# Kernel optimization log

Hardware: AMD Instinct MI355X
Metric: run time of the kernel (lower is better)

The kernel has to match this reference:

```python
import jax, jax.numpy as jnp
import numpy as np
import math

B, S, H, E, D = 4, 4096, 2048, 64, 256
ROUND_COUNT = 3
TARGET_APPLIED_FRACTION = 0.25


def setup_inputs() -> dict:
    key = jax.random.key(0)
    ks = jax.random.split(key, 10)
    sc = 0.02
    return {
        "hidden": jax.random.normal(ks[0], (B, S, H), jnp.float32),
        "W_ts": jax.random.normal(ks[1], (D, H), jnp.float32) * sc,
        "b_ts": jnp.zeros((D,), jnp.float32),
        "W_tr": jax.random.normal(ks[2], (E, H), jnp.float32) * sc,
        "b_tr": jnp.zeros((E,), jnp.float32),
        "W_sr": jax.random.normal(ks[3], (E, D), jnp.float32) * sc,
        "W_fb": jax.random.normal(ks[4], (D, E), jnp.float32) * sc,
        "W_r": jax.random.normal(ks[5], (D, D), jnp.float32) * sc,
        "b_r": jnp.zeros((D,), jnp.float32),
        "W_z": jax.random.normal(ks[6], (D, D), jnp.float32) * sc,
        "b_z": jnp.zeros((D,), jnp.float32),
        "W_ci": jax.random.normal(ks[7], (D, D), jnp.float32) * sc,
        "b_ci": jnp.zeros((D,), jnp.float32),
        "W_cs": jax.random.normal(ks[8], (D, D), jnp.float32) * sc,
    }


def _lowest_margin_fraction_mask(route_weights, frac):
    # winner margin: top1 - top2 over experts
    top2 = jax.lax.top_k(route_weights, 2)[0]          # [B,S,2]
    margins = top2[..., 0] - top2[..., 1]              # [B,S]
    flat = margins.reshape(-1)
    n = flat.shape[0]
    k = min(n, max(1, math.ceil(frac * n)))            # static count
    order = jnp.argsort(flat, stable=True)
    active = jnp.zeros((n,), jnp.bool_).at[order[:k]].set(True)
    return active.reshape(margins.shape)


def reference(hidden, W_ts, b_ts, W_tr, b_tr, W_sr, W_fb, W_r, b_r, W_z, b_z, W_ci, b_ci, W_cs):
    # token state + base route logits
    token_state = jnp.tanh(hidden @ W_ts.T + b_ts)          # [B,S,D]
    pooled_token_state = token_state.mean(axis=1, keepdims=True)  # [B,1,D]
    base_logits = hidden @ W_tr.T + b_tr                    # [B,S,E]

    controller = jnp.zeros((hidden.shape[0], 1, W_ts.shape[0]), hidden.dtype)  # [B,1,D]

    expert_logits = base_logits
    expert_weights = jax.nn.softmax(expert_logits, axis=-1)

    for round_index in range(ROUND_COUNT):
        if round_index > 0:
            # margin-gated conditional per-token update
            active = _lowest_margin_fraction_mask(expert_weights, TARGET_APPLIED_FRACTION)  # [B,S]
            state_route_bias = controller @ W_sr.T           # [B,1,E]
            candidate_logits = base_logits + state_route_bias
            expert_logits = jnp.where(active[..., None], candidate_logits, expert_logits)
            expert_weights = jax.nn.softmax(expert_logits, axis=-1)
        # GRU-style controller state update from pooled route feedback
        pooled_feedback = expert_weights.mean(axis=1, keepdims=True) @ W_fb.T  # [B,1,D]
        state_input = pooled_token_state + pooled_feedback
        reset_gate = jax.nn.sigmoid(state_input @ W_r.T + b_r)
        update_gate = jax.nn.sigmoid(state_input @ W_z.T + b_z)
        candidate_state = jnp.tanh(state_input @ W_ci.T + b_ci + (reset_gate * controller) @ W_cs.T)
        controller = (1.0 - update_gate) * controller + update_gate * candidate_state

    return expert_weights
```

## Files before the change

### kernel.cpp

```cpp
#include <hip/hip_runtime.h>
#include <hip/hip_bf16.h>
#include <math.h>

typedef unsigned int uint;
typedef unsigned short ushort_t;
typedef unsigned char uchar;

typedef __attribute__((ext_vector_type(4))) float f4_t;
typedef __attribute__((ext_vector_type(4))) ushort_t u16x4_t;
typedef __attribute__((ext_vector_type(4))) uint u32x4_t;
typedef __attribute__((ext_vector_type(8))) short bfrag_t;
typedef __attribute__((ext_vector_type(4))) float facc_t;

#define K_DIM 2048
#define D_DIM 256
#define E_DIM 64
#define N_DIM 320
#define S_DIM 4096
#define NTOK 16384
#define KSEL 4096

__device__ __forceinline__ ushort_t f2bf(float f) {
  uint u = __float_as_uint(f);
  uint r = u + 0x7FFFu + ((u >> 16) & 1u);
  return (ushort_t)(r >> 16);
}

__global__ __launch_bounds__(256) void prep_kernel(
    const float* __restrict__ W_ts, const float* __restrict__ W_tr,
    ushort_t* __restrict__ Wc, float* __restrict__ zero_region)
{
  int idx = blockIdx.x * 256 + threadIdx.x;
  if (idx < (N_DIM * K_DIM / 4)) {
    int n = idx >> 9;
    int k4 = (idx & 511) * 4;
    const float* src = (n < D_DIM) ? (W_ts + (size_t)n * K_DIM + k4)
                                   : (W_tr + (size_t)(n - D_DIM) * K_DIM + k4);
    f4_t v = *reinterpret_cast<const f4_t*>(src);
    u16x4_t h;
    h[0] = f2bf(v[0]); h[1] = f2bf(v[1]); h[2] = f2bf(v[2]); h[3] = f2bf(v[3]);
    *reinterpret_cast<u16x4_t*>(&Wc[(size_t)n * K_DIM + k4]) = h;
  }
  if (blockIdx.x == 0) {
    for (int i = threadIdx.x; i < 2560; i += 256) zero_region[i] = 0.f;
  }
}

#define BM 64
#define BK 64
#define LDK 72

__global__ __launch_bounds__(640, 2) void gemm_kernel(
    const float* __restrict__ hidden, const ushort_t* __restrict__ Wc,
    const float* __restrict__ b_ts, const float* __restrict__ b_tr,
    float* __restrict__ base_logits, float* __restrict__ pooled_ts)
{
  __shared__ ushort_t Alds[BM * LDK];
  __shared__ ushort_t Blds[N_DIM * LDK];
  const int tid = threadIdx.x;
  const int lane = tid & 63;
  const int w = tid >> 6;
  const int wc = w % 5;
  const int wrr = w / 5;
  const int row0 = blockIdx.x * BM;
  const int lr = lane & 15;
  const int lgp = lane >> 4;
  const bool hasA2 = (tid < 384);

  const int ar0 = tid >> 4, ac0 = (tid & 15) * 4;
  const int ar1 = (tid + 640) >> 4, ac1 = ((tid + 640) & 15) * 4;

  facc_t acc[2][4];
#pragma unroll
  for (int mi = 0; mi < 2; mi++)
#pragma unroll
    for (int ni = 0; ni < 4; ni++) acc[mi][ni] = (facc_t){0.f, 0.f, 0.f, 0.f};

  f4_t vaA0, vaA1;
  u32x4_t vb0_0, vb0_1, vb0_2, vb0_3;
  f4_t vaB0, vaB1;
  u32x4_t vb1_0, vb1_1, vb1_2, vb1_3;

#define LOAD_TILE(k0, vA0, vA1, b0, b1, b2, b3)                                  \
  {                                                                              \
    vA0 = *reinterpret_cast<const f4_t*>(hidden + (size_t)(row0 + ar0) * K_DIM + (k0) + ac0); \
    if (hasA2)                                                                   \
      vA1 = *reinterpret_cast<const f4_t*>(hidden + (size_t)(row0 + ar1) * K_DIM + (k0) + ac1); \
    b0 = *reinterpret_cast<const u32x4_t*>(Wc + (size_t)(tid >> 3) * K_DIM + (k0) + (tid & 7) * 8); \
    b1 = *reinterpret_cast<const u32x4_t*>(Wc + (size_t)((tid + 640) >> 3) * K_DIM + (k0) + ((tid + 640) & 7) * 8); \
    b2 = *reinterpret_cast<const u32x4_t*>(Wc + (size_t)((tid + 1280) >> 3) * K_DIM + (k0) + ((tid + 1280) & 7) * 8); \
    b3 = *reinterpret_cast<const u32x4_t*>(Wc + (size_t)((tid + 1920) >> 3) * K_DIM + (k0) + ((tid + 1920) & 7) * 8); \
  }

#define STORE_TILE(vA0, vA1, b0, b1, b2, b3)                                     \
  {                                                                              \
    u16x4_t h;                                                                   \
    h[0] = f2bf(vA0[0]); h[1] = f2bf(vA0[1]); h[2] = f2bf(vA0[2]); h[3] = f2bf(vA0[3]); \
    *reinterpret_cast<u16x4_t*>(&Alds[ar0 * LDK + ac0]) = h;                     \
    if (hasA2) {                                                                 \
      h[0] = f2bf(vA1[0]); h[1] = f2bf(vA1[1]); h[2] = f2bf(vA1[2]); h[3] = f2bf(vA1[3]); \
      *reinterpret_cast<u16x4_t*>(&Alds[ar1 * LDK + ac1]) = h;                   \
    }                                                                            \
    *reinterpret_cast<u32x4_t*>(&Blds[(tid >> 3) * LDK + (tid & 7) * 8]) = b0;   \
    *reinterpret_cast<u32x4_t*>(&Blds[((tid + 640) >> 3) * LDK + ((tid + 640) & 7) * 8]) = b1; \
    *reinterpret_cast<u32x4_t*>(&Blds[((tid + 1280) >> 3) * LDK + ((tid + 1280) & 7) * 8]) = b2; \
    *reinterpret_cast<u32x4_t*>(&Blds[((tid + 1920) >> 3) * LDK + ((tid + 1920) & 7) * 8]) = b3; \
  }

#define COMPUTE_TILE()                                                           \
  {                                                                              \
    _Pragma("unroll")                                                            \
    for (int kk = 0; kk < 2; ++kk) {                                             \
      bfrag_t af[2], bfv[4];                                                     \
      _Pragma("unroll")                                                          \
      for (int mi = 0; mi < 2; mi++)                                             \
        af[mi] = *reinterpret_cast<const bfrag_t*>(&Alds[(wrr * 32 + mi * 16 + lr) * LDK + kk * 32 + lgp * 8]); \
      _Pragma("unroll")                                                          \
      for (int ni = 0; ni < 4; ni++)                                             \
        bfv[ni] = *reinterpret_cast<const bfrag_t*>(&Blds[(wc * 64 + ni * 16 + lr) * LDK + kk * 32 + lgp * 8]); \
      _Pragma("unroll")                                                          \
      for (int mi = 0; mi < 2; mi++)                                             \
        _Pragma("unroll")                                                        \
        for (int ni = 0; ni < 4; ni++)                                           \
          acc[mi][ni] = __builtin_amdgcn_mfma_f32_16x16x32_bf16(af[mi], bfv[ni], acc[mi][ni], 0, 0, 0); \
    }                                                                            \
  }

  LOAD_TILE(0, vaA0, vaA1, vb0_0, vb0_1, vb0_2, vb0_3);

#pragma unroll 1
  for (int t = 0; t < 32; t += 2) {
    __syncthreads();
    STORE_TILE(vaA0, vaA1, vb0_0, vb0_1, vb0_2, vb0_3);
    LOAD_TILE((t + 1) * BK, vaB0, vaB1, vb1_0, vb1_1, vb1_2, vb1_3);
    __syncthreads();
    COMPUTE_TILE();

    __syncthreads();
    STORE_TILE(vaB0, vaB1, vb1_0, vb1_1, vb1_2, vb1_3);
    if (t + 2 < 32) LOAD_TILE((t + 2) * BK, vaA0, vaA1, vb0_0, vb0_1, vb0_2, vb0_3);
    __syncthreads();
    COMPUTE_TILE();
  }

  const int b = row0 >> 12;
  if (wc < 4) {
#pragma unroll
    for (int ni = 0; ni < 4; ni++) {
      const int col = wc * 64 + ni * 16 + lr;
      const float bias = b_ts[col];
      float psum = 0.f;
#pragma unroll
      for (int mi = 0; mi < 2; mi++)
#pragma unroll
        for (int j = 0; j < 4; j++)
          psum += tanhf(acc[mi][ni][j] + bias);
      psum += __shfl_xor(psum, 16, 64);
      psum += __shfl_xor(psum, 32, 64);
      if (lgp == 0) atomicAdd(&pooled_ts[b * D_DIM + col], psum);
    }
  } else {
#pragma unroll
    for (int ni = 0; ni < 4; ni++) {
      const int e = ni * 16 + lr;
      const float bias = b_tr[e];
#pragma unroll
      for (int mi = 0; mi < 2; mi++)
#pragma unroll
        for (int j = 0; j < 4; j++) {
          const int row = row0 + wrr * 32 + mi * 16 + lgp * 4 + j;
          base_logits[(size_t)row * E_DIM + e] = acc[mi][ni][j] + bias;
        }
    }
  }
}

__global__ __launch_bounds__(256) void route_kernel(
    int round,
    const float* __restrict__ base_logits,
    const float* __restrict__ bias1, const float* __restrict__ bias2,
    const uchar* __restrict__ active, uchar* __restrict__ tag,
    float* __restrict__ margins, float* __restrict__ pw_out,
    float* __restrict__ out)
{
  __shared__ float sm[4][64];
  const int tid = threadIdx.x;
  const int lane = tid & 63;
  const int wid = tid >> 6;
  const int b = blockIdx.x >> 8;
  const int t0 = blockIdx.x * 16 + wid * 4;

  float bv1 = 0.f, bv2 = 0.f;
  if (round >= 1) bv1 = bias1[b * E_DIM + lane];
  if (round == 2) bv2 = bias2[b * E_DIM + lane];

  float lg[4];
#pragma unroll
  for (int i = 0; i < 4; ++i)
    lg[i] = base_logits[(size_t)(t0 + i) * E_DIM + lane];

  if (round == 1) {
    uchar a[4];
#pragma unroll
    for (int i = 0; i < 4; ++i) a[i] = active[t0 + i];
#pragma unroll
    for (int i = 0; i < 4; ++i) {
      if (lane == 0) tag[t0 + i] = a[i];
      if (a[i]) lg[i] += bv1;
    }
  } else if (round == 2) {
    uchar a[4], tg[4];
#pragma unroll
    for (int i = 0; i < 4; ++i) { a[i] = active[t0 + i]; tg[i] = tag[t0 + i]; }
#pragma unroll
    for (int i = 0; i < 4; ++i)
      lg[i] += a[i] ? bv2 : (tg[i] ? bv1 : 0.f);
  }

  float pacc = 0.f;
#pragma unroll
  for (int i = 0; i < 4; ++i) {
    const float lgt = lg[i];
    float m1 = lgt;
#pragma unroll
    for (int mm = 32; mm; mm >>= 1) m1 = fmaxf(m1, __shfl_xor(m1, mm, 64));
    float e = expf(lgt - m1);
    float s = e;
#pragma unroll
    for (int mm = 32; mm; mm >>= 1) s += __shfl_xor(s, mm, 64);
    if (round == 2) {
      out[(size_t)(t0 + i) * E_DIM + lane] = e / s;
    } else {
      pacc += e / s;
      unsigned long long bal = __ballot(lgt == m1);
      int first = __ffsll((unsigned long long)bal) - 1;
      float l2 = (lane == first) ? -__builtin_inff() : lgt;
#pragma unroll
      for (int mm = 32; mm; mm >>= 1) l2 = fmaxf(l2, __shfl_xor(l2, mm, 64));
      if (lane == 0) margins[t0 + i] = (1.f - expf(l2 - m1)) / s;
    }
  }
  if (round != 2) {
    sm[wid][lane] = pacc;
    __syncthreads();
    if (wid == 0) {
      float v = sm[0][lane] + sm[1][lane] + sm[2][lane] + sm[3][lane];
      atomicAdd(&pw_out[b * E_DIM + lane], v);
    }
  }
}

__global__ __launch_bounds__(1024) void mid_kernel(
    const float* __restrict__ margins,
    const float* __restrict__ pw,
    const float* __restrict__ W_fb, const float* __restrict__ W_r, const float* __restrict__ b_r,
    const float* __restrict__ W_z, const float* __restrict__ b_z,
    const float* __restrict__ W_ci, const float* __restrict__ b_ci,
    const float* __restrict__ W_cs, const float* __restrict__ W_sr,
    const float* __restrict__ pooled_ts, float* __restrict__ ctrl,
    float* __restrict__ bias_out, uchar* __restrict__ active)
{
  const int tid = threadIdx.x;
  const int lane = tid & 63;
  const int wid = tid >> 6;
  if (blockIdx.x < 4) {
    __shared__ float si[256], rcs[256], zgs[256], ais[256], cns[256], pwl[64];
    const int b = blockIdx.x;
    if (tid < 64) pwl[tid] = pw[b * 64 + tid];
    __syncthreads();
    if (tid < 256) {
      const float* wr = W_fb + tid * 64;
      float pv = pooled_ts[b * 256 + tid];
      float s = 0.f;
#pragma unroll
      for (int j = 0; j < 16; ++j) {
        f4_t wv = *reinterpret_cast<const f4_t*>(wr + j * 4);
        s += wv[0] * pwl[j * 4] + wv[1] * pwl[j * 4 + 1]
           + wv[2] * pwl[j * 4 + 2] + wv[3] * pwl[j * 4 + 3];
      }
      si[tid] = (pv + s) * (1.f / 4096.f);
    }
    __syncthreads();
    if (tid < 768) {
      const int m = tid >> 8, r = tid & 255;
      const float* wr = ((m == 0) ? W_r : (m == 1) ? W_z : W_ci) + r * 256;
      float cold = (m == 0) ? ctrl[b * 256 + r] : 0.f;
      float s = 0.f;
#pragma unroll 16
      for (int j = 0; j < 64; ++j) {
        f4_t wv = *reinterpret_cast<const f4_t*>(wr + j * 4);
        f4_t xv = *reinterpret_cast<const f4_t*>(&si[j * 4]);
        s += wv[0] * xv[0] + wv[1] * xv[1] + wv[2] * xv[2] + wv[3] * xv[3];
      }
      if (m == 0)      rcs[r] = cold / (1.f + expf(-(s + b_r[r])));
      else if (m == 1) zgs[r] = 1.f / (1.f + expf(-(s + b_z[r])));
      else             ais[r] = s + b_ci[r];
    }
    __syncthreads();
    if (tid < 256) {
      const float* wr = W_cs + tid * 256;
      float cold = ctrl[b * 256 + tid];
      float s = 0.f;
#pragma unroll 16
      for (int j = 0; j < 64; ++j) {
        f4_t wv = *reinterpret_cast<const f4_t*>(wr + j * 4);
        f4_t xv = *reinterpret_cast<const f4_t*>(&rcs[j * 4]);
        s += wv[0] * xv[0] + wv[1] * xv[1] + wv[2] * xv[2] + wv[3] * xv[3];
      }
      float zg = zgs[tid];
      float cnew = (1.f - zg) * cold + zg * tanhf(ais[tid] + s);
      ctrl[b * 256 + tid] = cnew;
      cns[tid] = cnew;
    }
    __syncthreads();
    if (tid < 256) {
      const int r = tid >> 2, q = tid & 3;
      const float* wr = W_sr + r * 256 + q * 64;
      float s = 0.f;
#pragma unroll
      for (int j = 0; j < 16; ++j) {
        f4_t wv = *reinterpret_cast<const f4_t*>(wr + j * 4);
        f4_t xv = *reinterpret_cast<const f4_t*>(&cns[q * 64 + j * 4]);
        s += wv[0] * xv[0] + wv[1] * xv[1] + wv[2] * xv[2] + wv[3] * xv[3];
      }
      s += __shfl_xor(s, 1, 64);
      s += __shfl_xor(s, 2, 64);
      if (q == 0) bias_out[b * 64 + r] = s;
    }
  } else {
    __shared__ uint hist[256];
    __shared__ uint aux2[4];
    __shared__ uint wsum[16];
    const u32x4_t* mv = reinterpret_cast<const u32x4_t*>(margins);
    u32x4_t loc[4];
#pragma unroll
    for (int q = 0; q < 4; ++q) loc[q] = mv[tid * 4 + q];
    uint pfx = 0, kk = KSEL;
    for (int shift = 24; shift >= 0; shift -= 8) {
      if (tid < 256) hist[tid] = 0;
      __syncthreads();
#pragma unroll
      for (int q = 0; q < 4; ++q) {
#pragma unroll
        for (int e = 0; e < 4; ++e) {
          uint u = loc[q][e];
          bool ok = (shift == 24) || ((u >> (shift + 8)) == (pfx >> (shift + 8)));
          uint bin = (u >> shift) & 255u;
          unsigned long long m = __ballot(ok);
#pragma unroll
          for (int bit = 0; bit < 8; ++bit) {
            unsigned long long bb = __ballot(ok && ((bin >> bit) & 1u));
            m &= ((bin >> bit) & 1u) ? bb : ~bb;
          }
          if (ok && (__ffsll(m) - 1) == lane) atomicAdd(&hist[bin], (uint)__popcll(m));
        }
      }
      __syncthreads();
      uint hv = 0, hx = 0;
      if (tid < 256) {
        hv = hist[tid];
        hx = hv;
#pragma unroll
        for (int d = 1; d < 64; d <<= 1) {
          uint y = __shfl_up(hx, d, 64);
          if (lane >= d) hx += y;
        }
        if (lane == 63) wsum[wid] = hx;
      }
      __syncthreads();
      if (tid < 256) {
        uint base = 0;
        for (int w2 = 0; w2 < 4; ++w2) base += (w2 < wid) ? wsum[w2] : 0u;
        uint inc = hx + base;
        if (inc >= kk && (inc - hv) < kk) { aux2[0] = (uint)tid; aux2[1] = kk - (inc - hv); }
      }
      __syncthreads();
      pfx |= aux2[0] << shift;
      kk = aux2[1];
      __syncthreads();
    }
    const uint tval = pfx;
    if (tid == 0) aux2[2] = 0;
    __syncthreads();
    uint myLt = 0, myEq = 0;
#pragma unroll
    for (int q = 0; q < 4; ++q) {
#pragma unroll
      for (int e = 0; e < 4; ++e) {
        uint u = loc[q][e];
        myLt += (u < tval) ? 1u : 0u;
        myEq += (u == tval) ? 1u : 0u;
      }
    }
    uint lt = myLt;
#pragma unroll
    for (int m = 32; m; m >>= 1) lt += __shfl_xor(lt, m, 64);
    if (lane == 0) atomicAdd(&aux2[2], lt);
    uint x = myEq;
#pragma unroll
    for (int d = 1; d < 64; d <<= 1) {
      uint y = __shfl_up(x, d, 64);
      if (lane >= d) x += y;
    }
    if (lane == 63) wsum[wid] = x;
    __syncthreads();
    if (tid == 0) {
      uint run = 0;
      for (int w2 = 0; w2 < 16; ++w2) { uint c = wsum[w2]; wsum[w2] = run; run += c; }
      aux2[3] = (uint)KSEL - aux2[2];
    }
    __syncthreads();
    uint pos = wsum[wid] + (x - myEq);
    const uint need = aux2[3];
#pragma unroll
    for (int q = 0; q < 4; ++q) {
#pragma unroll
      for (int e = 0; e < 4; ++e) {
        uint u = loc[q][e];
        uchar a = 0;
        if (u < tval) a = 1;
        else if (u == tval) { a = (pos < need) ? 1 : 0; pos++; }
        active[tid * 16 + q * 4 + e] = a;
      }
    }
  }
}

extern "C" void kernel_launch(void* const* d_in, const int* in_sizes, int n_in,
                              void* d_out, int out_size, void* d_ws, size_t ws_size,
                              hipStream_t stream) {
  const float* hidden = (const float*)d_in[0];
  const float* W_ts = (const float*)d_in[1];
  const float* b_ts = (const float*)d_in[2];
  const float* W_tr = (const float*)d_in[3];
  const float* b_tr = (const float*)d_in[4];
  const float* W_sr = (const float*)d_in[5];
  const float* W_fb = (const float*)d_in[6];
  const float* W_r  = (const float*)d_in[7];
  const float* b_r  = (const float*)d_in[8];
  const float* W_z  = (const float*)d_in[9];
  const float* b_z  = (const float*)d_in[10];
  const float* W_ci = (const float*)d_in[11];
  const float* b_ci = (const float*)d_in[12];
  const float* W_cs = (const float*)d_in[13];
  float* out = (float*)d_out;

  char* ws = (char*)d_ws;
  float* base_logits = (float*)(ws);
  ushort_t* Wc = (ushort_t*)(ws + (4u << 20));
  float* margins = (float*)(ws + (4u << 20) + 1310720u);
  uchar* active = (uchar*)(ws + (4u << 20) + 1310720u + 65536u);
  uchar* tag    = (uchar*)(ws + (4u << 20) + 1310720u + 65536u + 16384u);
  float* pooled_ts = (float*)(ws + (4u << 20) + 1310720u + 65536u + 32768u);
  float* pw0   = pooled_ts + 1024;
  float* pw1   = pw0 + 256;
  float* ctrl  = pw1 + 256;
  float* bias1 = ctrl + 1024;
  float* bias2 = bias1 + 256;

  prep_kernel<<<640, 256, 0, stream>>>(W_ts, W_tr, Wc, pooled_ts);
  gemm_kernel<<<256, 640, 0, stream>>>(hidden, Wc, b_ts, b_tr, base_logits, pooled_ts);
  route_kernel<<<1024, 256, 0, stream>>>(0, base_logits, nullptr, nullptr, nullptr, nullptr,
                                         margins, pw0, nullptr);
  mid_kernel<<<5, 1024, 0, stream>>>(margins, pw0, W_fb, W_r, b_r, W_z, b_z, W_ci, b_ci,
                                     W_cs, W_sr, pooled_ts, ctrl, bias1, active);
  route_kernel<<<1024, 256, 0, stream>>>(1, base_logits, bias1, nullptr, active, tag,
                                         margins, pw1, nullptr);
  mid_kernel<<<5, 1024, 0, stream>>>(margins, pw1, W_fb, W_r, b_r, W_z, b_z, W_ci, b_ci,
                                     W_cs, W_sr, pooled_ts, ctrl, bias2, active);
  route_kernel<<<1024, 256, 0, stream>>>(2, base_logits, bias1, bias2, active, tag,
                                         nullptr, nullptr, out);
}
```

Measured before the change: 350.3 us.

## Halve GEMM row tile and split GRU controller update into parallel kernels

The GEMM block shrinks from 64 to 32 rows with 320 threads, doubling the grid to 512 blocks so more CUs are occupied, though each block reloads the full weight tile for fewer rows. The single 5-block mid kernel, which ran the GRU chain serially per batch within one block, is split into a feedback/select kernel plus three small kernels (gates, candidate, route bias). These spread the matvecs over more blocks with 4-lane partial dot products. The cost is extra kernel launches and global-memory round trips for the intermediate vectors.

```diff
diff --git a/kernel.cpp b/kernel.cpp
--- a/kernel.cpp
+++ b/kernel.cpp
@@ -24,6 +24,10 @@
   uint u = __float_as_uint(f);
   uint r = u + 0x7FFFu + ((u >> 16) & 1u);
   return (ushort_t)(r >> 16);
+}
+
+__device__ __forceinline__ float dot4(f4_t a, f4_t b) {
+  return a[0] * b[0] + a[1] * b[1] + a[2] * b[2] + a[3] * b[3];
 }
 
 __global__ __launch_bounds__(256) void prep_kernel(
@@ -46,11 +50,11 @@
   }
 }
 
-#define BM 64
+#define BM 32
 #define BK 64
 #define LDK 72
 
-__global__ __launch_bounds__(640, 2) void gemm_kernel(
+__global__ __launch_bounds__(320, 2) void gemm_kernel(
     const float* __restrict__ hidden, const ushort_t* __restrict__ Wc,
     const float* __restrict__ b_ts, const float* __restrict__ b_tr,
     float* __restrict__ base_logits, float* __restrict__ pooled_ts)
@@ -59,16 +63,14 @@
   __shared__ ushort_t Blds[N_DIM * LDK];
   const int tid = threadIdx.x;
   const int lane = tid & 63;
-  const int w = tid >> 6;
-  const int wc = w % 5;
-  const int wrr = w / 5;
+  const int wc = tid >> 6;
   const int row0 = blockIdx.x * BM;
   const int lr = lane & 15;
   const int lgp = lane >> 4;
-  const bool hasA2 = (tid < 384);
+  const bool hasA2 = (tid < 192);
 
   const int ar0 = tid >> 4, ac0 = (tid & 15) * 4;
-  const int ar1 = (tid + 640) >> 4, ac1 = ((tid + 640) & 15) * 4;
+  const int ar1 = (tid + 320) >> 4, ac1 = ((tid + 320) & 15) * 4;
 
   facc_t acc[2][4];
 #pragma unroll
@@ -77,22 +79,25 @@
     for (int ni = 0; ni < 4; ni++) acc[mi][ni] = (facc_t){0.f, 0.f, 0.f, 0.f};
 
   f4_t vaA0, vaA1;
-  u32x4_t vb0_0, vb0_1, vb0_2, vb0_3;
+  u32x4_t bA0, bA1, bA2, bA3, bA4, bA5, bA6, bA7;
   f4_t vaB0, vaB1;
-  u32x4_t vb1_0, vb1_1, vb1_2, vb1_3;
-
-#define LOAD_TILE(k0, vA0, vA1, b0, b1, b2, b3)                                  \
+  u32x4_t bB0, bB1, bB2, bB3, bB4, bB5, bB6, bB7;
+
+#define BLD(k0, kk2) *reinterpret_cast<const u32x4_t*>( \
+    Wc + (size_t)((tid + (kk2) * 320) >> 3) * K_DIM + (k0) + ((tid + (kk2) * 320) & 7) * 8)
+#define BST(kk2, reg) *reinterpret_cast<u32x4_t*>( \
+    &Blds[((tid + (kk2) * 320) >> 3) * LDK + ((tid + (kk2) * 320) & 7) * 8]) = reg
+
+#define LOAD_TILE(k0, vA0, vA1, b0, b1, b2, b3, b4, b5, b6, b7)                  \
   {                                                                              \
     vA0 = *reinterpret_cast<const f4_t*>(hidden + (size_t)(row0 + ar0) * K_DIM + (k0) + ac0); \
     if (hasA2)                                                                   \
       vA1 = *reinterpret_cast<const f4_t*>(hidden + (size_t)(row0 + ar1) * K_DIM + (k0) + ac1); \
-    b0 = *reinterpret_cast<const u32x4_t*>(Wc + (size_t)(tid >> 3) * K_DIM + (k0) + (tid & 7) * 8); \
-    b1 = *reinterpret_cast<const u32x4_t*>(Wc + (size_t)((tid + 640) >> 3) * K_DIM + (k0) + ((tid + 640) & 7) * 8); \
-    b2 = *reinterpret_cast<const u32x4_t*>(Wc + (size_t)((tid + 1280) >> 3) * K_DIM + (k0) + ((tid + 1280) & 7) * 8); \
-    b3 = *reinterpret_cast<const u32x4_t*>(Wc + (size_t)((tid + 1920) >> 3) * K_DIM + (k0) + ((tid + 1920) & 7) * 8); \
-  }
-
-#define STORE_TILE(vA0, vA1, b0, b1, b2, b3)                                     \
+    b0 = BLD(k0, 0); b1 = BLD(k0, 1); b2 = BLD(k0, 2); b3 = BLD(k0, 3);          \
+    b4 = BLD(k0, 4); b5 = BLD(k0, 5); b6 = BLD(k0, 6); b7 = BLD(k0, 7);          \
+  }
+
+#define STORE_TILE(vA0, vA1, b0, b1, b2, b3, b4, b5, b6, b7)                     \
   {                                                                              \
     u16x4_t h;                                                                   \
     h[0] = f2bf(vA0[0]); h[1] = f2bf(vA0[1]); h[2] = f2bf(vA0[2]); h[3] = f2bf(vA0[3]); \
@@ -101,10 +106,8 @@
       h[0] = f2bf(vA1[0]); h[1] = f2bf(vA1[1]); h[2] = f2bf(vA1[2]); h[3] = f2bf(vA1[3]); \
       *reinterpret_cast<u16x4_t*>(&Alds[ar1 * LDK + ac1]) = h;                   \
     }                                                                            \
-    *reinterpret_cast<u32x4_t*>(&Blds[(tid >> 3) * LDK + (tid & 7) * 8]) = b0;   \
-    *reinterpret_cast<u32x4_t*>(&Blds[((tid + 640) >> 3) * LDK + ((tid + 640) & 7) * 8]) = b1; \
-    *reinterpret_cast<u32x4_t*>(&Blds[((tid + 1280) >> 3) * LDK + ((tid + 1280) & 7) * 8]) = b2; \
-    *reinterpret_cast<u32x4_t*>(&Blds[((tid + 1920) >> 3) * LDK + ((tid + 1920) & 7) * 8]) = b3; \
+    BST(0, b0); BST(1, b1); BST(2, b2); BST(3, b3);                              \
+    BST(4, b4); BST(5, b5); BST(6, b6); BST(7, b7);                              \
   }
 
 #define COMPUTE_TILE()                                                           \
@@ -114,7 +117,7 @@
       bfrag_t af[2], bfv[4];                                                     \
       _Pragma("unroll")                                                          \
       for (int mi = 0; mi < 2; mi++)                                             \
-        af[mi] = *reinterpret_cast<const bfrag_t*>(&Alds[(wrr * 32 + mi * 16 + lr) * LDK + kk * 32 + lgp * 8]); \
+        af[mi] = *reinterpret_cast<const bfrag_t*>(&Alds[(mi * 16 + lr) * LDK + kk * 32 + lgp * 8]); \
       _Pragma("unroll")                                                          \
       for (int ni = 0; ni < 4; ni++)                                             \
         bfv[ni] = *reinterpret_cast<const bfrag_t*>(&Blds[(wc * 64 + ni * 16 + lr) * LDK + kk * 32 + lgp * 8]); \
@@ -126,19 +129,20 @@
     }                                                                            \
   }
 
-  LOAD_TILE(0, vaA0, vaA1, vb0_0, vb0_1, vb0_2, vb0_3);
+  LOAD_TILE(0, vaA0, vaA1, bA0, bA1, bA2, bA3, bA4, bA5, bA6, bA7);
 
 #pragma unroll 1
   for (int t = 0; t < 32; t += 2) {
     __syncthreads();
-    STORE_TILE(vaA0, vaA1, vb0_0, vb0_1, vb0_2, vb0_3);
-    LOAD_TILE((t + 1) * BK, vaB0, vaB1, vb1_0, vb1_1, vb1_2, vb1_3);
+    STORE_TILE(vaA0, vaA1, bA0, bA1, bA2, bA3, bA4, bA5, bA6, bA7);
+    LOAD_TILE((t + 1) * BK, vaB0, vaB1, bB0, bB1, bB2, bB3, bB4, bB5, bB6, bB7);
     __syncthreads();
     COMPUTE_TILE();
 
     __syncthreads();
-    STORE_TILE(vaB0, vaB1, vb1_0, vb1_1, vb1_2, vb1_3);
-    if (t + 2 < 32) LOAD_TILE((t + 2) * BK, vaA0, vaA1, vb0_0, vb0_1, vb0_2, vb0_3);
+    STORE_TILE(vaB0, vaB1, bB0, bB1, bB2, bB3, bB4, bB5, bB6, bB7);
+    if (t + 2 < 32)
+      LOAD_TILE((t + 2) * BK, vaA0, vaA1, bA0, bA1, bA2, bA3, bA4, bA5, bA6, bA7);
     __syncthreads();
     COMPUTE_TILE();
   }
@@ -168,7 +172,7 @@
       for (int mi = 0; mi < 2; mi++)
 #pragma unroll
         for (int j = 0; j < 4; j++) {
-          const int row = row0 + wrr * 32 + mi * 16 + lgp * 4 + j;
+          const int row = row0 + mi * 16 + lgp * 4 + j;
           base_logits[(size_t)row * E_DIM + e] = acc[mi][ni][j] + bias;
         }
     }
@@ -250,82 +254,45 @@
   }
 }
 
-__global__ __launch_bounds__(1024) void mid_kernel(
-    const float* __restrict__ margins,
-    const float* __restrict__ pw,
-    const float* __restrict__ W_fb, const float* __restrict__ W_r, const float* __restrict__ b_r,
-    const float* __restrict__ W_z, const float* __restrict__ b_z,
-    const float* __restrict__ W_ci, const float* __restrict__ b_ci,
-    const float* __restrict__ W_cs, const float* __restrict__ W_sr,
-    const float* __restrict__ pooled_ts, float* __restrict__ ctrl,
-    float* __restrict__ bias_out, uchar* __restrict__ active)
+
+__global__ __launch_bounds__(1024) void midA_kernel(
+    const float* __restrict__ margins, const float* __restrict__ pw,
+    const float* __restrict__ W_fb, const float* __restrict__ pooled_ts,
+    float* __restrict__ si_buf, uchar* __restrict__ active)
 {
   const int tid = threadIdx.x;
   const int lane = tid & 63;
   const int wid = tid >> 6;
   if (blockIdx.x < 4) {
-    __shared__ float si[256], rcs[256], zgs[256], ais[256], cns[256], pwl[64];
-    const int b = blockIdx.x;
-    if (tid < 64) pwl[tid] = pw[b * 64 + tid];
+    __shared__ __align__(16) float pwl[256];
+    if (tid < 256) pwl[tid] = pw[tid];
     __syncthreads();
     if (tid < 256) {
-      const float* wr = W_fb + tid * 64;
-      float pv = pooled_ts[b * 256 + tid];
-      float s = 0.f;
-#pragma unroll
-      for (int j = 0; j < 16; ++j) {
-        f4_t wv = *reinterpret_cast<const f4_t*>(wr + j * 4);
-        s += wv[0] * pwl[j * 4] + wv[1] * pwl[j * 4 + 1]
-           + wv[2] * pwl[j * 4 + 2] + wv[3] * pwl[j * 4 + 3];
-      }
-      si[tid] = (pv + s) * (1.f / 4096.f);
-    }
-    __syncthreads();
-    if (tid < 768) {
-      const int m = tid >> 8, r = tid & 255;
-      const float* wr = ((m == 0) ? W_r : (m == 1) ? W_z : W_ci) + r * 256;
-      float cold = (m == 0) ? ctrl[b * 256 + r] : 0.f;
-      float s = 0.f;
-#pragma unroll 16
-      for (int j = 0; j < 64; ++j) {
-        f4_t wv = *reinterpret_cast<const f4_t*>(wr + j * 4);
-        f4_t xv = *reinterpret_cast<const f4_t*>(&si[j * 4]);
-        s += wv[0] * xv[0] + wv[1] * xv[1] + wv[2] * xv[2] + wv[3] * xv[3];
-      }
-      if (m == 0)      rcs[r] = cold / (1.f + expf(-(s + b_r[r])));
-      else if (m == 1) zgs[r] = 1.f / (1.f + expf(-(s + b_z[r])));
-      else             ais[r] = s + b_ci[r];
-    }
-    __syncthreads();
-    if (tid < 256) {
-      const float* wr = W_cs + tid * 256;
-      float cold = ctrl[b * 256 + tid];
-      float s = 0.f;
-#pragma unroll 16
-      for (int j = 0; j < 64; ++j) {
-        f4_t wv = *reinterpret_cast<const f4_t*>(wr + j * 4);
-        f4_t xv = *reinterpret_cast<const f4_t*>(&rcs[j * 4]);
-        s += wv[0] * xv[0] + wv[1] * xv[1] + wv[2] * xv[2] + wv[3] * xv[3];
-      }
-      float zg = zgs[tid];
-      float cnew = (1.f - zg) * cold + zg * tanhf(ais[tid] + s);
-      ctrl[b * 256 + tid] = cnew;
-      cns[tid] = cnew;
-    }
-    __syncthreads();
-    if (tid < 256) {
-      const int r = tid >> 2, q = tid & 3;
-      const float* wr = W_sr + r * 256 + q * 64;
-      float s = 0.f;
-#pragma unroll
-      for (int j = 0; j < 16; ++j) {
-        f4_t wv = *reinterpret_cast<const f4_t*>(wr + j * 4);
-        f4_t xv = *reinterpret_cast<const f4_t*>(&cns[q * 64 + j * 4]);
-        s += wv[0] * xv[0] + wv[1] * xv[1] + wv[2] * xv[2] + wv[3] * xv[3];
-      }
-      s += __shfl_xor(s, 1, 64);
-      s += __shfl_xor(s, 2, 64);
-      if (q == 0) bias_out[b * 64 + r] = s;
+      const int r = blockIdx.x * 64 + (tid >> 2), q = tid & 3;
+      const float* wr = W_fb + r * 64 + q * 16;
+      f4_t w0 = *reinterpret_cast<const f4_t*>(wr);
+      f4_t w1 = *reinterpret_cast<const f4_t*>(wr + 4);
+      f4_t w2 = *reinterpret_cast<const f4_t*>(wr + 8);
+      f4_t w3 = *reinterpret_cast<const f4_t*>(wr + 12);
+      float sb[4];
+#pragma unroll
+      for (int b2 = 0; b2 < 4; ++b2) {
+        const float* xb = &pwl[b2 * 64 + q * 16];
+        sb[b2] = dot4(w0, *reinterpret_cast<const f4_t*>(xb))
+               + dot4(w1, *reinterpret_cast<const f4_t*>(xb + 4))
+               + dot4(w2, *reinterpret_cast<const f4_t*>(xb + 8))
+               + dot4(w3, *reinterpret_cast<const f4_t*>(xb + 12));
+      }
+#pragma unroll
+      for (int b2 = 0; b2 < 4; ++b2) {
+        sb[b2] += __shfl_xor(sb[b2], 1, 64);
+        sb[b2] += __shfl_xor(sb[b2], 2, 64);
+      }
+      if (q == 0) {
+#pragma unroll
+        for (int b2 = 0; b2 < 4; ++b2)
+          si_buf[b2 * 256 + r] = (pooled_ts[b2 * 256 + r] + sb[b2]) * (1.f / 4096.f);
+      }
     }
   } else {
     __shared__ uint hist[256];
@@ -423,6 +390,123 @@
         active[tid * 16 + q * 4 + e] = a;
       }
     }
+  }
+}
+
+__global__ __launch_bounds__(256) void gru2_kernel(
+    const float* __restrict__ W_r, const float* __restrict__ W_z,
+    const float* __restrict__ W_ci, const float* __restrict__ b_r,
+    const float* __restrict__ b_z, const float* __restrict__ b_ci,
+    const float* __restrict__ si_buf, const float* __restrict__ ctrl,
+    float* __restrict__ rcs_buf, float* __restrict__ zgs_buf,
+    float* __restrict__ ais_buf)
+{
+  __shared__ __align__(16) float sil[1024];
+  const int tid = threadIdx.x;
+  for (int i = tid; i < 1024; i += 256) sil[i] = si_buf[i];
+  __syncthreads();
+  const int m = blockIdx.x >> 2;
+  const int r = (blockIdx.x & 3) * 64 + (tid >> 2), q = tid & 3;
+  const float* wr = ((m == 0) ? W_r : (m == 1) ? W_z : W_ci) + r * 256 + q * 64;
+  float s0 = 0.f, s1 = 0.f, s2 = 0.f, s3 = 0.f;
+#pragma unroll
+  for (int j = 0; j < 16; ++j) {
+    f4_t wv = *reinterpret_cast<const f4_t*>(wr + j * 4);
+    s0 += dot4(wv, *reinterpret_cast<const f4_t*>(&sil[q * 64 + j * 4]));
+    s1 += dot4(wv, *reinterpret_cast<const f4_t*>(&sil[256 + q * 64 + j * 4]));
+    s2 += dot4(wv, *reinterpret_cast<const f4_t*>(&sil[512 + q * 64 + j * 4]));
+    s3 += dot4(wv, *reinterpret_cast<const f4_t*>(&sil[768 + q * 64 + j * 4]));
+  }
+  s0 += __shfl_xor(s0, 1, 64); s0 += __shfl_xor(s0, 2, 64);
+  s1 += __shfl_xor(s1, 1, 64); s1 += __shfl_xor(s1, 2, 64);
+  s2 += __shfl_xor(s2, 1, 64); s2 += __shfl_xor(s2, 2, 64);
+  s3 += __shfl_xor(s3, 1, 64); s3 += __shfl_xor(s3, 2, 64);
+  if (q == 0) {
+    float sv[4] = {s0, s1, s2, s3};
+    if (m == 0) {
+      const float bb = b_r[r];
+#pragma unroll
+      for (int b2 = 0; b2 < 4; ++b2)
+        rcs_buf[b2 * 256 + r] = ctrl[b2 * 256 + r] / (1.f + expf(-(sv[b2] + bb)));
+    } else if (m == 1) {
+      const float bb = b_z[r];
+#pragma unroll
+      for (int b2 = 0; b2 < 4; ++b2)
+        zgs_buf[b2 * 256 + r] = 1.f / (1.f + expf(-(sv[b2] + bb)));
+    } else {
+      const float bb = b_ci[r];
+#pragma unroll
+      for (int b2 = 0; b2 < 4; ++b2)
+        ais_buf[b2 * 256 + r] = sv[b2] + bb;
+    }
+  }
+}
+
+__global__ __launch_bounds__(256) void gru3_kernel(
+    const float* __restrict__ W_cs, const float* __restrict__ rcs_buf,
+    const float* __restrict__ zgs_buf, const float* __restrict__ ais_buf,
+    float* __restrict__ ctrl, float* __restrict__ cns_buf)
+{
+  __shared__ __align__(16) float rl[1024];
+  const int tid = threadIdx.x;
+  for (int i = tid; i < 1024; i += 256) rl[i] = rcs_buf[i];
+  __syncthreads();
+  const int r = blockIdx.x * 64 + (tid >> 2), q = tid & 3;
+  const float* wr = W_cs + r * 256 + q * 64;
+  float s0 = 0.f, s1 = 0.f, s2 = 0.f, s3 = 0.f;
+#pragma unroll
+  for (int j = 0; j < 16; ++j) {
+    f4_t wv = *reinterpret_cast<const f4_t*>(wr + j * 4);
+    s0 += dot4(wv, *reinterpret_cast<const f4_t*>(&rl[q * 64 + j * 4]));
+    s1 += dot4(wv, *reinterpret_cast<const f4_t*>(&rl[256 + q * 64 + j * 4]));
+    s2 += dot4(wv, *reinterpret_cast<const f4_t*>(&rl[512 + q * 64 + j * 4]));
+    s3 += dot4(wv, *reinterpret_cast<const f4_t*>(&rl[768 + q * 64 + j * 4]));
+  }
+  s0 += __shfl_xor(s0, 1, 64); s0 += __shfl_xor(s0, 2, 64);
+  s1 += __shfl_xor(s1, 1, 64); s1 += __shfl_xor(s1, 2, 64);
+  s2 += __shfl_xor(s2, 1, 64); s2 += __shfl_xor(s2, 2, 64);
+  s3 += __shfl_xor(s3, 1, 64); s3 += __shfl_xor(s3, 2, 64);
+  if (q == 0) {
+    float sv[4] = {s0, s1, s2, s3};
+#pragma unroll
+    for (int b2 = 0; b2 < 4; ++b2) {
+      float cold = ctrl[b2 * 256 + r];
+      float zg = zgs_buf[b2 * 256 + r];
+      float cnew = (1.f - zg) * cold + zg * tanhf(ais_buf[b2 * 256 + r] + sv[b2]);
+      ctrl[b2 * 256 + r] = cnew;
+      cns_buf[b2 * 256 + r] = cnew;
+    }
+  }
+}
+
+__global__ __launch_bounds__(256) void gru4_kernel(
+    const float* __restrict__ W_sr, const float* __restrict__ cns_buf,
+    float* __restrict__ bias_out)
+{
+  __shared__ __align__(16) float cl[1024];
+  const int tid = threadIdx.x;
+  for (int i = tid; i < 1024; i += 256) cl[i] = cns_buf[i];
+  __syncthreads();
+  const int r = tid >> 2, q = tid & 3;
+  const float* wr = W_sr + r * 256 + q * 64;
+  float s0 = 0.f, s1 = 0.f, s2 = 0.f, s3 = 0.f;
+#pragma unroll
+  for (int j = 0; j < 16; ++j) {
+    f4_t wv = *reinterpret_cast<const f4_t*>(wr + j * 4);
+    s0 += dot4(wv, *reinterpret_cast<const f4_t*>(&cl[q * 64 + j * 4]));
+    s1 += dot4(wv, *reinterpret_cast<const f4_t*>(&cl[256 + q * 64 + j * 4]));
+    s2 += dot4(wv, *reinterpret_cast<const f4_t*>(&cl[512 + q * 64 + j * 4]));
+    s3 += dot4(wv, *reinterpret_cast<const f4_t*>(&cl[768 + q * 64 + j * 4]));
+  }
+  s0 += __shfl_xor(s0, 1, 64); s0 += __shfl_xor(s0, 2, 64);
+  s1 += __shfl_xor(s1, 1, 64); s1 += __shfl_xor(s1, 2, 64);
+  s2 += __shfl_xor(s2, 1, 64); s2 += __shfl_xor(s2, 2, 64);
+  s3 += __shfl_xor(s3, 1, 64); s3 += __shfl_xor(s3, 2, 64);
+  if (q == 0) {
+    bias_out[r]       = s0;
+    bias_out[64 + r]  = s1;
+    bias_out[128 + r] = s2;
+    bias_out[192 + r] = s3;
   }
 }
 
@@ -457,17 +541,28 @@
   float* ctrl  = pw1 + 256;
   float* bias1 = ctrl + 1024;
   float* bias2 = bias1 + 256;
+  float* si_buf  = bias2 + 256;
+  float* rcs_buf = si_buf + 1024;
+  float* zgs_buf = rcs_buf + 1024;
+  float* ais_buf = zgs_buf + 1024;
+  float* cns_buf = ais_buf + 1024;
 
   prep_kernel<<<640, 256, 0, stream>>>(W_ts, W_tr, Wc, pooled_ts);
-  gemm_kernel<<<256, 640, 0, stream>>>(hidden, Wc, b_ts, b_tr, base_logits, pooled_ts);
+  gemm_kernel<<<512, 320, 0, stream>>>(hidden, Wc, b_ts, b_tr, base_logits, pooled_ts);
   route_kernel<<<1024, 256, 0, stream>>>(0, base_logits, nullptr, nullptr, nullptr, nullptr,
                                          margins, pw0, nullptr);
-  mid_kernel<<<5, 1024, 0, stream>>>(margins, pw0, W_fb, W_r, b_r, W_z, b_z, W_ci, b_ci,
-                                     W_cs, W_sr, pooled_ts, ctrl, bias1, active);
+  midA_kernel<<<5, 1024, 0, stream>>>(margins, pw0, W_fb, pooled_ts, si_buf, active);
+  gru2_kernel<<<12, 256, 0, stream>>>(W_r, W_z, W_ci, b_r, b_z, b_ci, si_buf, ctrl,
+                                      rcs_buf, zgs_buf, ais_buf);
+  gru3_kernel<<<4, 256, 0, stream>>>(W_cs, rcs_buf, zgs_buf, ais_buf, ctrl, cns_buf);
+  gru4_kernel<<<1, 256, 0, stream>>>(W_sr, cns_buf, bias1);
   route_kernel<<<1024, 256, 0, stream>>>(1, base_logits, bias1, nullptr, active, tag,
                                          margins, pw1, nullptr);
-  mid_kernel<<<5, 1024, 0, stream>>>(margins, pw1, W_fb, W_r, b_r, W_z, b_z, W_ci, b_ci,
-                                     W_cs, W_sr, pooled_ts, ctrl, bias2, active);
+  midA_kernel<<<5, 1024, 0, stream>>>(margins, pw1, W_fb, pooled_ts, si_buf, active);
+  gru2_kernel<<<12, 256, 0, stream>>>(W_r, W_z, W_ci, b_r, b_z, b_ci, si_buf, ctrl,
+                                      rcs_buf, zgs_buf, ais_buf);
+  gru3_kernel<<<4, 256, 0, stream>>>(W_cs, rcs_buf, zgs_buf, ais_buf, ctrl, cns_buf);
+  gru4_kernel<<<1, 256, 0, stream>>>(W_sr, cns_buf, bias2);
   route_kernel<<<1024, 256, 0, stream>>>(2, base_logits, bias1, bias2, active, tag,
                                          nullptr, nullptr, out);
 }
```

Measured after the change: 399.6 us. 1.14x slower.
